# Performance work log

Hardware: AMD Instinct MI355X
Metric: run time of the kernel (lower is better)

## Reference

```python
import jax, jax.numpy as jnp
import numpy as np

C = 256
CK = C // 8  # key/query channels


def setup_inputs() -> dict:
    key = jax.random.key(0)
    ks = jax.random.split(key, 7)
    B, H, W = 8, 64, 64
    x = jax.random.normal(ks[0], (B, C, H, W), dtype=jnp.float32)
    # 1x1 conv weights (out_ch, in_ch) and biases. Spectral norm is a weight
    # reparameterization; at forward time it is just a conv with (normalized)
    # weights, so we sample weights directly.
    Wf = jax.random.normal(ks[1], (CK, C), dtype=jnp.float32) * 0.02
    bf = jnp.zeros((CK,), dtype=jnp.float32)
    Wg = jax.random.normal(ks[2], (CK, C), dtype=jnp.float32) * 0.02
    bg = jnp.zeros((CK,), dtype=jnp.float32)
    Wh = jax.random.normal(ks[3], (C, C), dtype=jnp.float32) * 0.02
    bh = jnp.zeros((C,), dtype=jnp.float32)
    gamma = jnp.ones((1,), dtype=jnp.float32) * 0.5  # nonzero so attention path matters
    return {"x": x, "Wf": Wf, "bf": bf, "Wg": Wg, "bg": bg, "Wh": Wh, "bh": bh, "gamma": gamma}


def reference(x, Wf, bf, Wg, bg, Wh, bh, gamma):
    b, c, h, w = x.shape
    n = h * w
    xf = x.reshape(b, c, n)  # [B, C, N]
    # 1x1 convs == per-pixel linear maps
    fx = jnp.einsum("kc,bcn->bkn", Wf, xf) + bf[None, :, None]  # [B, CK, N]
    gx = jnp.einsum("kc,bcn->bkn", Wg, xf) + bg[None, :, None]  # [B, CK, N]
    hx = jnp.einsum("oc,bcn->bon", Wh, xf) + bh[None, :, None]  # [B, C, N]
    # sx[b, i, j] = <fx[:, i], gx[:, j]>
    sx = jnp.einsum("bki,bkj->bij", fx, gx)  # [B, N, N]
    # torch F.softmax(sx, dim=1): normalize over the first N axis (i)
    beta = jax.nn.softmax(sx, axis=1)
    ox = jnp.einsum("bci,bij->bcj", hx, beta).reshape(b, c, h, w)
    return gamma.reshape(()) * ox + x
```

## Files before the change

### kernel.cpp

```cpp
#include <hip/hip_runtime.h>
#include <stdint.h>


typedef __bf16 bf16;
typedef __bf16 bf16x2 __attribute__((ext_vector_type(2)));
typedef __bf16 bf16x8 __attribute__((ext_vector_type(8)));
typedef float  f32x16 __attribute__((ext_vector_type(16)));
typedef float  f32x4  __attribute__((ext_vector_type(4)));

#define BATCH 8
#define CC    256
#define CKK   32
#define NN    4096
#define LOG2E 1.4426950408889634f

__device__ __forceinline__ f32x16 zero16() {
  f32x16 z;
#pragma unroll
  for (int i = 0; i < 16; ++i) z[i] = 0.0f;
  return z;
}

__device__ __forceinline__ unsigned pack2(float lo, float hi) {
  bf16x2 v = {(bf16)lo, (bf16)hi};
  return __builtin_bit_cast(unsigned, v);
}

__device__ __forceinline__ f32x16 mfma32(bf16x8 a, bf16x8 b, f32x16 c) {
  return __builtin_amdgcn_mfma_f32_32x32x16_bf16(a, b, c, 0, 0, 0);
}

#define GLDS16(srcp, dstp)                                                         \
  __builtin_amdgcn_global_load_lds(                                               \
      (const __attribute__((address_space(1))) void*)(srcp),                      \
      (__attribute__((address_space(3))) void*)(dstp), 16, 0, 0)

__global__ __launch_bounds__(256) void k_transpose(const float* __restrict__ x,
                                                   bf16* __restrict__ xT) {
  __shared__ float tile[64][65];
  const int n0 = blockIdx.x * 64;
  const int c0 = blockIdx.y * 64;
  const int b  = blockIdx.z;
  const int t = threadIdx.x;
  const int tn = t & 63, trow = t >> 6;
#pragma unroll
  for (int i = 0; i < 16; ++i) {
    int c = trow + i * 4;
    tile[c][tn] = x[((size_t)(b * CC + c0 + c)) * NN + n0 + tn];
  }
  __syncthreads();
#pragma unroll
  for (int i = 0; i < 16; ++i) {
    int n = trow + i * 4;
    xT[((size_t)(b * NN + n0 + n)) * CC + c0 + tn] = (bf16)tile[tn][n];
  }
}

__global__ __launch_bounds__(64) void k_wprep(const float* __restrict__ Wf, const float* __restrict__ bfv,
                                              const float* __restrict__ Wg, const float* __restrict__ bg,
                                              const float* __restrict__ Wh, const float* __restrict__ bh,
                                              bf16* __restrict__ Wcat, float* __restrict__ bcat) {
  const int ko = blockIdx.x;
  const int t = threadIdx.x;
  const float* src;
  float scale = 1.0f;
  if (ko < 32) src = Wf + (size_t)ko * CC;
  else if (ko < 64) { src = Wg + (size_t)(ko - 32) * CC; scale = LOG2E; }
  else src = Wh + (size_t)(ko - 64) * CC;
#pragma unroll
  for (int i = 0; i < 4; ++i)
    Wcat[(size_t)ko * CC + t + i * 64] = (bf16)(src[t + i * 64] * scale);
  if (ko == 0) {
    for (int i = t; i < 320; i += 64) {
      float v = (i < 32) ? bfv[i] : (i < 64) ? bg[i - 32] * LOG2E : bh[i - 64];
      bcat[i] = v;
    }
  }
}

__global__ __launch_bounds__(256, 1) void k_proj(const bf16* __restrict__ xT,
                                                 const bf16* __restrict__ Wcat,
                                                 const float* __restrict__ bcat,
                                                 bf16* __restrict__ fxT, bf16* __restrict__ gxT,
                                                 bf16* __restrict__ hx) {
  const int d = blockIdx.x;
  const int b = d & 7, nb = d >> 3;
  const int t = threadIdx.x;
  const int w = t >> 6, ln = t & 63, ln31 = ln & 31, h = ln >> 5;
  const int n = nb * 128 + w * 32 + ln31;

  f32x16 acc[10];
#pragma unroll
  for (int mt = 0; mt < 10; ++mt) acc[mt] = zero16();

  const bf16* xrow = xT + ((size_t)(b * NN + n)) * CC;
#pragma unroll
  for (int ks = 0; ks < 16; ++ks) {
    bf16x8 bfrag = *(const bf16x8*)(xrow + ks * 16 + h * 8);
#pragma unroll
    for (int mt = 0; mt < 10; ++mt) {
      bf16x8 afrag = *(const bf16x8*)(Wcat + (size_t)(mt * 32 + ln31) * CC + ks * 16 + h * 8);
      acc[mt] = mfma32(afrag, bfrag, acc[mt]);
    }
  }

#pragma unroll
  for (int mt = 0; mt < 10; ++mt) {
#pragma unroll
    for (int q = 0; q < 4; ++q) {
      const int ko0 = mt * 32 + 8 * q + 4 * h;
      float v0 = acc[mt][4 * q + 0] + bcat[ko0 + 0];
      float v1 = acc[mt][4 * q + 1] + bcat[ko0 + 1];
      float v2 = acc[mt][4 * q + 2] + bcat[ko0 + 2];
      float v3 = acc[mt][4 * q + 3] + bcat[ko0 + 3];
      if (mt < 2) {
        bf16* dst = (mt == 0 ? fxT : gxT) + ((size_t)(b * NN + n)) * CKK + (8 * q + 4 * h);
        uint2 pv;
        pv.x = pack2(v0, v1);
        pv.y = pack2(v2, v3);
        *(uint2*)dst = pv;
      } else {
        const int c = ko0 - 64;
        hx[((size_t)(b * CC + c + 0)) * NN + n] = (bf16)v0;
        hx[((size_t)(b * CC + c + 1)) * NN + n] = (bf16)v1;
        hx[((size_t)(b * CC + c + 2)) * NN + n] = (bf16)v2;
        hx[((size_t)(b * CC + c + 3)) * NN + n] = (bf16)v3;
      }
    }
  }
}

__global__ __launch_bounds__(512, 2) void k_attn(const bf16* __restrict__ fxT,
                                                 const bf16* __restrict__ gxT,
                                                 const bf16* __restrict__ hx,
                                                 const float* __restrict__ x,
                                                 const float* __restrict__ gammap,
                                                 float* __restrict__ out) {
  extern __shared__ __align__(16) char smem[];
  __shared__ float lsh[128];
  const int d = blockIdx.x;
  const int b = d & 7, jb = d >> 3;
  const int t = threadIdx.x;
  const int g = t >> 8;
  const int tg = t & 255;
  const int wg = tg >> 6;
  const int ln = t & 63, ln31 = ln & 31, h = ln >> 5;
  const int j = jb * 128 + wg * 32 + ln31;
  const int kbase = g * 2048;

  const bf16* fxb = fxT + (size_t)b * NN * CKK;
  const bf16* hxb = hx + (size_t)b * CC * NN;

  bf16* vsg = (bf16*)smem + g * 32768;
  bf16* ksg = (bf16*)(smem + 131072) + g * 6144;

  const bf16* qrow = gxT + ((size_t)b * NN + j) * CKK;
  bf16x8 qf0 = *(const bf16x8*)(qrow + h * 8);
  bf16x8 qf1 = *(const bf16x8*)(qrow + 16 + h * 8);
  asm volatile("" ::: "memory");

  int voff[4];
#pragma unroll
  for (int ks = 0; ks < 4; ++ks)
    voff[ks] = ln31 * 64 + (((2 * ks + h) ^ (ln31 & 7)) * 8);
  const int tk = (ln31 >> 1) & 3;
  const int ko0 = ln31 * 32 + ((h ^ tk) * 8);
  const int ko1 = ln31 * 32 + (((2 + h) ^ tk) * 8);

  const int vrow_l = ln >> 3;
  const int vcol_l = ((ln & 7) ^ ((ln >> 3) & 7)) * 8;
  const bf16* vlane = hxb + (size_t)(wg * 64 + vrow_l) * NN + vcol_l;
  const int krow_l = ln >> 2;
  const int kcol_l = ((ln & 3) ^ ((ln >> 3) & 3)) * 8;
  const bf16* klane = fxb + (size_t)(wg * 16 + krow_l) * CKK + kcol_l;

#define STAGEV(slot, i0s)                                                     \
  {                                                                            \
    _Pragma("unroll")                                                          \
    for (int q = 0; q < 8; ++q)                                                \
      GLDS16(vlane + (size_t)q * 8 * NN + (i0s),                               \
             vsg + (slot) * 16384 + (wg * 64 + q * 8) * 64);                   \
  }
#define STAGEK(kslot, i0s)                                                    \
  { GLDS16(klane + (size_t)(i0s) * CKK, ksg + (kslot) * 2048 + wg * 16 * 32); }

  f32x16 oacc[8];
#pragma unroll
  for (int ct = 0; ct < 8; ++ct) oacc[ct] = zero16();
  float l_run = 0.0f;
  bf16x8 pf[4] = {};

  auto QK = [&](int kslot, f32x16& s0, f32x16& s1) {
    const bf16* kt = ksg + kslot * 2048;
    bf16x8 kf00 = *(const bf16x8*)(kt + ko0);
    bf16x8 kf01 = *(const bf16x8*)(kt + ko1);
    bf16x8 kf10 = *(const bf16x8*)(kt + 1024 + ko0);
    bf16x8 kf11 = *(const bf16x8*)(kt + 1024 + ko1);
    s0 = zero16(); s1 = zero16();
    s0 = mfma32(kf00, qf0, s0);
    s0 = mfma32(kf01, qf1, s0);
    s1 = mfma32(kf10, qf0, s1);
    s1 = mfma32(kf11, qf1, s1);
  };
  auto SM = [&](const f32x16& s0, const f32x16& s1) {
    float ls0 = 0.0f, ls1 = 0.0f, ls2 = 0.0f, ls3 = 0.0f;
    unsigned pk0[4][2], pk1[4][2];
#pragma unroll
    for (int q = 0; q < 4; ++q)
#pragma unroll
      for (int wi = 0; wi < 2; ++wi) {
        float a0 = __builtin_exp2f(s0[4 * q + 2 * wi]);
        float a1 = __builtin_exp2f(s0[4 * q + 2 * wi + 1]);
        float b0 = __builtin_exp2f(s1[4 * q + 2 * wi]);
        float b1 = __builtin_exp2f(s1[4 * q + 2 * wi + 1]);
        ls0 += a0; ls1 += a1; ls2 += b0; ls3 += b1;
        pk0[q][wi] = pack2(a0, a1);
        pk1[q][wi] = pack2(b0, b1);
      }
    l_run += (ls0 + ls1) + (ls2 + ls3);
#pragma unroll
    for (int ks = 0; ks < 2; ++ks) {
      union { unsigned u[4]; bf16x8 v; } pa, pb;
#pragma unroll
      for (int wi = 0; wi < 2; ++wi) {
        unsigned x0 = pk0[2 * ks][wi],     y0 = pk0[2 * ks + 1][wi];
        asm("v_permlane32_swap_b32 %0, %1" : "+v"(x0), "+v"(y0));
        pa.u[wi] = x0; pa.u[2 + wi] = y0;
        unsigned x1 = pk1[2 * ks][wi],     y1 = pk1[2 * ks + 1][wi];
        asm("v_permlane32_swap_b32 %0, %1" : "+v"(x1), "+v"(y1));
        pb.u[wi] = x1; pb.u[2 + wi] = y1;
      }
      pf[ks] = pa.v;
      pf[2 + ks] = pb.v;
    }
  };
  auto PV = [&](int slot) {
    const bf16* vb = vsg + slot * 16384;
    bf16x8 va0, va1, va2, va3, vn0, vn1, vn2, vn3;
    va0 = *(const bf16x8*)(vb + voff[0]);
    va1 = *(const bf16x8*)(vb + voff[1]);
    va2 = *(const bf16x8*)(vb + voff[2]);
    va3 = *(const bf16x8*)(vb + voff[3]);
    __builtin_amdgcn_s_setprio(1);
#pragma unroll
    for (int ct = 0; ct < 8; ++ct) {
      if (ct < 7) {
        const bf16* vrow = vb + (ct + 1) * 2048;
        vn0 = *(const bf16x8*)(vrow + voff[0]);
        vn1 = *(const bf16x8*)(vrow + voff[1]);
        vn2 = *(const bf16x8*)(vrow + voff[2]);
        vn3 = *(const bf16x8*)(vrow + voff[3]);
      }
      oacc[ct] = mfma32(va0, pf[0], oacc[ct]);
      oacc[ct] = mfma32(va1, pf[1], oacc[ct]);
      oacc[ct] = mfma32(va2, pf[2], oacc[ct]);
      oacc[ct] = mfma32(va3, pf[3], oacc[ct]);
      va0 = vn0; va1 = vn1; va2 = vn2; va3 = vn3;
    }
    __builtin_amdgcn_s_setprio(0);
  };

  STAGEV(0, kbase);
  STAGEK(0, kbase);
  STAGEK(1, kbase + 64);

  for (int kb = 0; kb < 32; ++kb) {
    asm volatile("s_waitcnt vmcnt(0)" ::: "memory");
    __builtin_amdgcn_s_barrier();
    asm volatile("" ::: "memory");

    f32x16 s0, s1;
    if (g == 0) {
      QK(kb % 3, s0, s1);
      SM(s0, s1);
    } else if (kb > 0) {
      PV((kb - 1) & 1);
    }

    __builtin_amdgcn_s_barrier();
    asm volatile("" ::: "memory");

    STAGEV((kb + 1) & 1, kbase + ((kb + 1) & 31) * 64);
    STAGEK((kb + 2) % 3, kbase + ((kb + 2) & 31) * 64);

    if (g == 0) {
      PV(kb & 1);
    } else {
      QK(kb % 3, s0, s1);
      SM(s0, s1);
    }
  }
  if (g == 1) PV(31 & 1);

  l_run += __shfl_xor(l_run, 32);

  asm volatile("s_waitcnt vmcnt(0) lgkmcnt(0)" ::: "memory");
  __builtin_amdgcn_s_barrier();
  asm volatile("" ::: "memory");

  float* obuf = (float*)smem;
  const int jl = wg * 32 + ln31;
  if (g == 1) {
#pragma unroll
    for (int ct = 0; ct < 8; ++ct)
#pragma unroll
      for (int q = 0; q < 4; ++q) {
        f32x4 v;
        v[0] = oacc[ct][4 * q + 0];
        v[1] = oacc[ct][4 * q + 1];
        v[2] = oacc[ct][4 * q + 2];
        v[3] = oacc[ct][4 * q + 3];
        *(f32x4*)&obuf[jl * 260 + ct * 32 + 8 * q + 4 * h] = v;
      }
    if (h == 0) lsh[jl] = l_run;
  }
  __syncthreads();
  if (g == 0) {
    const float l = l_run + lsh[jl];
    const float ginv = gammap[0] / l;
    const float* xb = x + (size_t)b * CC * NN;
    float* ob = out + (size_t)b * CC * NN;
#pragma unroll
    for (int ct = 0; ct < 8; ++ct)
#pragma unroll
      for (int q = 0; q < 4; ++q) {
        f32x4 vB = *(const f32x4*)&obuf[jl * 260 + ct * 32 + 8 * q + 4 * h];
#pragma unroll
        for (int s = 0; s < 4; ++s) {
          int c = ct * 32 + 8 * q + 4 * h + s;
          size_t idx = (size_t)c * NN + j;
          float val = oacc[ct][4 * q + s] + vB[s];
          ob[idx] = fmaf(ginv, val, xb[idx]);
        }
      }
  }
#undef STAGEV
#undef STAGEK
}

extern "C" void kernel_launch(void* const* d_in, const int* in_sizes, int n_in,
                              void* d_out, int out_size, void* d_ws, size_t ws_size,
                              hipStream_t stream) {
  const float* x     = (const float*)d_in[0];
  const float* Wf    = (const float*)d_in[1];
  const float* bfv   = (const float*)d_in[2];
  const float* Wg    = (const float*)d_in[3];
  const float* bg    = (const float*)d_in[4];
  const float* Wh    = (const float*)d_in[5];
  const float* bh    = (const float*)d_in[6];
  const float* gamma = (const float*)d_in[7];
  float* out = (float*)d_out;

  char* ws = (char*)d_ws;
  bf16* fxT  = (bf16*)(ws);
  bf16* gxT  = (bf16*)(ws + 2097152);
  bf16* hx   = (bf16*)(ws + 4194304);
  bf16* Wcat = (bf16*)(ws + 20971520);
  float* bcat = (float*)(ws + 21135360);
  bf16* xT = (bf16*)d_out;

  k_transpose<<<dim3(64, 4, 8), 256, 0, stream>>>(x, xT);
  k_wprep<<<dim3(320), 64, 0, stream>>>(Wf, bfv, Wg, bg, Wh, bh, Wcat, bcat);
  k_proj<<<dim3(256), 256, 0, stream>>>(xT, Wcat, bcat, fxT, gxT, hx);
  k_attn<<<dim3(256), 512, 155648, stream>>>(fxT, gxT, hx, x, gamma, out);
}
```

Before: 145.6 us.

## Use FP8 for value projection and softmax probabilities in PV matmul

Stores the value projection hx as FP8 instead of bf16, and converts the exponentiated attention scores to FP8, so the PV product runs on the fp8 32x32x16 MFMA. This halves V staging traffic and LDS footprint, and the LDS layout and swizzle are reworked for byte-sized elements. The price is lower precision in both operands of the dominant matmul. Unnormalized exp values (up to large magnitudes) quantized to e4m3 risk overflow or accuracy loss.

```diff
diff --git a/kernel.cpp b/kernel.cpp
--- a/kernel.cpp
+++ b/kernel.cpp
@@ -7,6 +7,8 @@
 typedef __bf16 bf16x8 __attribute__((ext_vector_type(8)));
 typedef float  f32x16 __attribute__((ext_vector_type(16)));
 typedef float  f32x4  __attribute__((ext_vector_type(4)));
+typedef unsigned char u8;
+typedef long   i64;
 
 #define BATCH 8
 #define CC    256
@@ -28,6 +30,10 @@
 
 __device__ __forceinline__ f32x16 mfma32(bf16x8 a, bf16x8 b, f32x16 c) {
   return __builtin_amdgcn_mfma_f32_32x32x16_bf16(a, b, c, 0, 0, 0);
+}
+
+__device__ __forceinline__ f32x16 mfma8(i64 a, i64 b, f32x16 c) {
+  return __builtin_amdgcn_mfma_f32_32x32x16_fp8_fp8(a, b, c, 0, 0, 0);
 }
 
 #define GLDS16(srcp, dstp)                                                         \
@@ -82,7 +88,7 @@
                                                  const bf16* __restrict__ Wcat,
                                                  const float* __restrict__ bcat,
                                                  bf16* __restrict__ fxT, bf16* __restrict__ gxT,
-                                                 bf16* __restrict__ hx) {
+                                                 u8* __restrict__ hx8) {
   const int d = blockIdx.x;
   const int b = d & 7, nb = d >> 3;
   const int t = threadIdx.x;
@@ -121,10 +127,13 @@
         *(uint2*)dst = pv;
       } else {
         const int c = ko0 - 64;
-        hx[((size_t)(b * CC + c + 0)) * NN + n] = (bf16)v0;
-        hx[((size_t)(b * CC + c + 1)) * NN + n] = (bf16)v1;
-        hx[((size_t)(b * CC + c + 2)) * NN + n] = (bf16)v2;
-        hx[((size_t)(b * CC + c + 3)) * NN + n] = (bf16)v3;
+        unsigned wpk = (unsigned)__builtin_amdgcn_cvt_pk_fp8_f32(v0, v1, 0, false);
+        wpk = (unsigned)__builtin_amdgcn_cvt_pk_fp8_f32(v2, v3, (int)wpk, true);
+        u8* hp = hx8 + ((size_t)(b * CC + c)) * NN + n;
+        hp[0]          = (u8)(wpk & 0xff);
+        hp[NN]         = (u8)((wpk >> 8) & 0xff);
+        hp[2 * NN]     = (u8)((wpk >> 16) & 0xff);
+        hp[3 * NN]     = (u8)(wpk >> 24);
       }
     }
   }
@@ -132,7 +141,7 @@
 
 __global__ __launch_bounds__(512, 2) void k_attn(const bf16* __restrict__ fxT,
                                                  const bf16* __restrict__ gxT,
-                                                 const bf16* __restrict__ hx,
+                                                 const u8* __restrict__ hx8,
                                                  const float* __restrict__ x,
                                                  const float* __restrict__ gammap,
                                                  float* __restrict__ out) {
@@ -149,27 +158,26 @@
   const int kbase = g * 2048;
 
   const bf16* fxb = fxT + (size_t)b * NN * CKK;
-  const bf16* hxb = hx + (size_t)b * CC * NN;
-
-  bf16* vsg = (bf16*)smem + g * 32768;
-  bf16* ksg = (bf16*)(smem + 131072) + g * 6144;
+  const u8*   hxb = hx8 + (size_t)b * CC * NN;
+
+  u8*   vsg = (u8*)smem + g * 32768;
+  bf16* ksg = (bf16*)(smem + 65536) + g * 6144;
 
   const bf16* qrow = gxT + ((size_t)b * NN + j) * CKK;
   bf16x8 qf0 = *(const bf16x8*)(qrow + h * 8);
   bf16x8 qf1 = *(const bf16x8*)(qrow + 16 + h * 8);
   asm volatile("" ::: "memory");
 
-  int voff[4];
+  int voff8[4];
 #pragma unroll
   for (int ks = 0; ks < 4; ++ks)
-    voff[ks] = ln31 * 64 + (((2 * ks + h) ^ (ln31 & 7)) * 8);
+    voff8[ks] = ln31 * 64 + (((ks + (ln31 >> 1)) & 3) * 16) + 8 * h;
   const int tk = (ln31 >> 1) & 3;
   const int ko0 = ln31 * 32 + ((h ^ tk) * 8);
   const int ko1 = ln31 * 32 + (((2 + h) ^ tk) * 8);
 
-  const int vrow_l = ln >> 3;
-  const int vcol_l = ((ln & 7) ^ ((ln >> 3) & 7)) * 8;
-  const bf16* vlane = hxb + (size_t)(wg * 64 + vrow_l) * NN + vcol_l;
+  const int vm = ((ln & 3) - (ln >> 3)) & 3;
+  const u8* vlane8 = hxb + (size_t)(wg * 64 + (ln >> 2)) * NN + vm * 16;
   const int krow_l = ln >> 2;
   const int kcol_l = ((ln & 3) ^ ((ln >> 3) & 3)) * 8;
   const bf16* klane = fxb + (size_t)(wg * 16 + krow_l) * CKK + kcol_l;
@@ -177,9 +185,9 @@
 #define STAGEV(slot, i0s)                                                     \
   {                                                                            \
     _Pragma("unroll")                                                          \
-    for (int q = 0; q < 8; ++q)                                                \
-      GLDS16(vlane + (size_t)q * 8 * NN + (i0s),                               \
-             vsg + (slot) * 16384 + (wg * 64 + q * 8) * 64);                   \
+    for (int q = 0; q < 4; ++q)                                                \
+      GLDS16(vlane8 + (size_t)q * 16 * NN + (i0s),                             \
+             vsg + (slot) * 16384 + (wg * 4 + q) * 1024);                      \
   }
 #define STAGEK(kslot, i0s)                                                    \
   { GLDS16(klane + (size_t)(i0s) * CKK, ksg + (kslot) * 2048 + wg * 16 * 32); }
@@ -188,7 +196,7 @@
 #pragma unroll
   for (int ct = 0; ct < 8; ++ct) oacc[ct] = zero16();
   float l_run = 0.0f;
-  bf16x8 pf[4] = {};
+  i64 pf[4] = {};
 
   auto QK = [&](int kslot, f32x16& s0, f32x16& s1) {
     const bf16* kt = ksg + kslot * 2048;
@@ -203,58 +211,59 @@
     s1 = mfma32(kf11, qf1, s1);
   };
   auto SM = [&](const f32x16& s0, const f32x16& s1) {
+    float e0[16], e1[16];
+#pragma unroll
+    for (int r = 0; r < 16; ++r) e0[r] = __builtin_exp2f(s0[r]);
+#pragma unroll
+    for (int r = 0; r < 16; ++r) e1[r] = __builtin_exp2f(s1[r]);
     float ls0 = 0.0f, ls1 = 0.0f, ls2 = 0.0f, ls3 = 0.0f;
-    unsigned pk0[4][2], pk1[4][2];
-#pragma unroll
-    for (int q = 0; q < 4; ++q)
-#pragma unroll
-      for (int wi = 0; wi < 2; ++wi) {
-        float a0 = __builtin_exp2f(s0[4 * q + 2 * wi]);
-        float a1 = __builtin_exp2f(s0[4 * q + 2 * wi + 1]);
-        float b0 = __builtin_exp2f(s1[4 * q + 2 * wi]);
-        float b1 = __builtin_exp2f(s1[4 * q + 2 * wi + 1]);
-        ls0 += a0; ls1 += a1; ls2 += b0; ls3 += b1;
-        pk0[q][wi] = pack2(a0, a1);
-        pk1[q][wi] = pack2(b0, b1);
-      }
+#pragma unroll
+    for (int r = 0; r < 4; ++r) {
+      ls0 += e0[r];      ls1 += e0[4 + r];
+      ls2 += e0[8 + r];  ls3 += e0[12 + r];
+      ls0 += e1[r];      ls1 += e1[4 + r];
+      ls2 += e1[8 + r];  ls3 += e1[12 + r];
+    }
     l_run += (ls0 + ls1) + (ls2 + ls3);
-#pragma unroll
-    for (int ks = 0; ks < 2; ++ks) {
-      union { unsigned u[4]; bf16x8 v; } pa, pb;
-#pragma unroll
-      for (int wi = 0; wi < 2; ++wi) {
-        unsigned x0 = pk0[2 * ks][wi],     y0 = pk0[2 * ks + 1][wi];
-        asm("v_permlane32_swap_b32 %0, %1" : "+v"(x0), "+v"(y0));
-        pa.u[wi] = x0; pa.u[2 + wi] = y0;
-        unsigned x1 = pk1[2 * ks][wi],     y1 = pk1[2 * ks + 1][wi];
-        asm("v_permlane32_swap_b32 %0, %1" : "+v"(x1), "+v"(y1));
-        pb.u[wi] = x1; pb.u[2 + wi] = y1;
-      }
-      pf[ks] = pa.v;
-      pf[2 + ks] = pb.v;
+    unsigned pk4[8];
+#pragma unroll
+    for (int A = 0; A < 4; ++A) {
+      unsigned w = (unsigned)__builtin_amdgcn_cvt_pk_fp8_f32(e0[4 * A], e0[4 * A + 1], 0, false);
+      pk4[A] = (unsigned)__builtin_amdgcn_cvt_pk_fp8_f32(e0[4 * A + 2], e0[4 * A + 3], (int)w, true);
+    }
+#pragma unroll
+    for (int A = 0; A < 4; ++A) {
+      unsigned w = (unsigned)__builtin_amdgcn_cvt_pk_fp8_f32(e1[4 * A], e1[4 * A + 1], 0, false);
+      pk4[4 + A] = (unsigned)__builtin_amdgcn_cvt_pk_fp8_f32(e1[4 * A + 2], e1[4 * A + 3], (int)w, true);
+    }
+#pragma unroll
+    for (int f = 0; f < 4; ++f) {
+      unsigned xw = pk4[2 * f], yw = pk4[2 * f + 1];
+      asm("v_permlane32_swap_b32 %0, %1" : "+v"(xw), "+v"(yw));
+      pf[f] = (i64)(((unsigned long long)yw << 32) | xw);
     }
   };
   auto PV = [&](int slot) {
-    const bf16* vb = vsg + slot * 16384;
-    bf16x8 va0, va1, va2, va3, vn0, vn1, vn2, vn3;
-    va0 = *(const bf16x8*)(vb + voff[0]);
-    va1 = *(const bf16x8*)(vb + voff[1]);
-    va2 = *(const bf16x8*)(vb + voff[2]);
-    va3 = *(const bf16x8*)(vb + voff[3]);
+    const u8* vb = vsg + slot * 16384;
+    i64 va0, va1, va2, va3, vn0, vn1, vn2, vn3;
+    va0 = *(const i64*)(vb + voff8[0]);
+    va1 = *(const i64*)(vb + voff8[1]);
+    va2 = *(const i64*)(vb + voff8[2]);
+    va3 = *(const i64*)(vb + voff8[3]);
     __builtin_amdgcn_s_setprio(1);
 #pragma unroll
     for (int ct = 0; ct < 8; ++ct) {
       if (ct < 7) {
-        const bf16* vrow = vb + (ct + 1) * 2048;
-        vn0 = *(const bf16x8*)(vrow + voff[0]);
-        vn1 = *(const bf16x8*)(vrow + voff[1]);
-        vn2 = *(const bf16x8*)(vrow + voff[2]);
-        vn3 = *(const bf16x8*)(vrow + voff[3]);
+        const u8* vrow = vb + (ct + 1) * 2048;
+        vn0 = *(const i64*)(vrow + voff8[0]);
+        vn1 = *(const i64*)(vrow + voff8[1]);
+        vn2 = *(const i64*)(vrow + voff8[2]);
+        vn3 = *(const i64*)(vrow + voff8[3]);
       }
-      oacc[ct] = mfma32(va0, pf[0], oacc[ct]);
-      oacc[ct] = mfma32(va1, pf[1], oacc[ct]);
-      oacc[ct] = mfma32(va2, pf[2], oacc[ct]);
-      oacc[ct] = mfma32(va3, pf[3], oacc[ct]);
+      oacc[ct] = mfma8(va0, pf[0], oacc[ct]);
+      oacc[ct] = mfma8(va1, pf[1], oacc[ct]);
+      oacc[ct] = mfma8(va2, pf[2], oacc[ct]);
+      oacc[ct] = mfma8(va3, pf[3], oacc[ct]);
       va0 = vn0; va1 = vn1; va2 = vn2; va3 = vn3;
     }
     __builtin_amdgcn_s_setprio(0);
@@ -354,13 +363,13 @@
   char* ws = (char*)d_ws;
   bf16* fxT  = (bf16*)(ws);
   bf16* gxT  = (bf16*)(ws + 2097152);
-  bf16* hx   = (bf16*)(ws + 4194304);
-  bf16* Wcat = (bf16*)(ws + 20971520);
-  float* bcat = (float*)(ws + 21135360);
+  u8*   hx8  = (u8*)(ws + 4194304);
+  bf16* Wcat = (bf16*)(ws + 12582912);
+  float* bcat = (float*)(ws + 12746752);
   bf16* xT = (bf16*)d_out;
 
   k_transpose<<<dim3(64, 4, 8), 256, 0, stream>>>(x, xT);
   k_wprep<<<dim3(320), 64, 0, stream>>>(Wf, bfv, Wg, bg, Wh, bh, Wcat, bcat);
-  k_proj<<<dim3(256), 256, 0, stream>>>(xT, Wcat, bcat, fxT, gxT, hx);
-  k_attn<<<dim3(256), 512, 155648, stream>>>(fxT, gxT, hx, x, gamma, out);
-}
+  k_proj<<<dim3(256), 256, 0, stream>>>(xT, Wcat, bcat, fxT, gxT, hx8);
+  k_attn<<<dim3(256), 512, 133120, stream>>>(fxT, gxT, hx8, x, gamma, out);
+}
```

After: 136.4 us. -6.3%, faster.
